# Kernel tuning notes

Hardware: AMD Instinct MI355X
Metric: run time of the kernel (lower is better)

## Reference

```python
import jax, jax.numpy as jnp
import numpy as np

NUM_LABELS = 512
MIN_INTENSITY = -0.003
MAX_INTENSITY = 0.003
BACKGROUND = 0


def setup_inputs() -> dict:
    key = jax.random.key(0)
    k1, k2 = jax.random.split(key)
    shape = (16, 1024, 1024)
    label_image = jax.random.randint(k1, shape, 0, NUM_LABELS, dtype=jnp.int32)
    intensity_image = jax.random.normal(k2, shape, dtype=jnp.float32)
    return {"label_image": label_image, "intensity_image": intensity_image}


def reference(label_image, intensity_image):
    # Single-pass segment reduce over all pixels, replacing the O(L*N) python loop.
    labels_flat = label_image.reshape(-1)
    vals_flat = intensity_image.reshape(-1)
    sums = jax.ops.segment_sum(vals_flat, labels_flat, num_segments=NUM_LABELS)
    counts = jax.ops.segment_sum(jnp.ones_like(vals_flat), labels_flat,
                                 num_segments=NUM_LABELS)
    means = sums / jnp.maximum(counts, 1.0)  # labels absent from image are never indexed
    label_ids = jnp.arange(NUM_LABELS, dtype=label_image.dtype)
    # Both min and max thresholds are set (truthy), background label is exempt.
    bad = ((means < MIN_INTENSITY) | (means > MAX_INTENSITY)) & (label_ids != BACKGROUND)
    # Threshold-based scatter filter: failing labels -> background.
    return jnp.where(bad[label_image], jnp.asarray(BACKGROUND, label_image.dtype), label_image)
```

## Files before the change

kernel.cpp:

```cpp
#include <hip/hip_runtime.h>

#define NUM_LABELS 512
#define MIN_INTENSITY (-0.003f)
#define MAX_INTENSITY (0.003f)


__global__ __launch_bounds__(256) void accum_kernel(
    const int* __restrict__ labels,
    const float* __restrict__ vals,
    float* __restrict__ g_sum,
    unsigned int* __restrict__ g_cnt,
    int n) {
  __shared__ float s_sum[NUM_LABELS];
  __shared__ unsigned int s_cnt[NUM_LABELS];
  for (int i = threadIdx.x; i < NUM_LABELS; i += blockDim.x) {
    s_sum[i] = 0.0f;
    s_cnt[i] = 0u;
  }
  __syncthreads();

  const int n4 = n >> 2;
  const int stride = gridDim.x * blockDim.x;
  int i = blockIdx.x * blockDim.x + threadIdx.x;
  const int4* l4 = reinterpret_cast<const int4*>(labels);
  const float4* v4 = reinterpret_cast<const float4*>(vals);
  for (; i < n4; i += stride) {
    int4 l = l4[i];
    float4 v = v4[i];
    atomicAdd(&s_sum[l.x], v.x); atomicAdd(&s_cnt[l.x], 1u);
    atomicAdd(&s_sum[l.y], v.y); atomicAdd(&s_cnt[l.y], 1u);
    atomicAdd(&s_sum[l.z], v.z); atomicAdd(&s_cnt[l.z], 1u);
    atomicAdd(&s_sum[l.w], v.w); atomicAdd(&s_cnt[l.w], 1u);
  }
  for (int t = (n4 << 2) + blockIdx.x * blockDim.x + threadIdx.x; t < n;
       t += stride) {
    atomicAdd(&s_sum[labels[t]], vals[t]);
    atomicAdd(&s_cnt[labels[t]], 1u);
  }
  __syncthreads();

  for (int j = threadIdx.x; j < NUM_LABELS; j += blockDim.x) {
    unsigned int c = s_cnt[j];
    if (c) {
      atomicAdd(&g_sum[j], s_sum[j]);
      atomicAdd(&g_cnt[j], c);
    }
  }
}

__global__ __launch_bounds__(NUM_LABELS) void flags_kernel(
    const float* __restrict__ g_sum,
    const unsigned int* __restrict__ g_cnt,
    int* __restrict__ bad) {
  int l = threadIdx.x;
  float c = (float)g_cnt[l];
  float mean = g_sum[l] / fmaxf(c, 1.0f);
  int b = ((mean < MIN_INTENSITY) || (mean > MAX_INTENSITY)) && (l != 0);
  bad[l] = b;
}

__global__ __launch_bounds__(256) void apply_kernel(
    const int* __restrict__ labels,
    const int* __restrict__ bad,
    int* __restrict__ out,
    int n) {
  __shared__ int s_bad[NUM_LABELS];
  for (int i = threadIdx.x; i < NUM_LABELS; i += blockDim.x)
    s_bad[i] = bad[i];
  __syncthreads();

  const int n4 = n >> 2;
  const int stride = gridDim.x * blockDim.x;
  int i = blockIdx.x * blockDim.x + threadIdx.x;
  const int4* l4 = reinterpret_cast<const int4*>(labels);
  int4* o4 = reinterpret_cast<int4*>(out);
  for (; i < n4; i += stride) {
    int4 l = l4[i];
    int4 o;
    o.x = s_bad[l.x] ? 0 : l.x;
    o.y = s_bad[l.y] ? 0 : l.y;
    o.z = s_bad[l.z] ? 0 : l.z;
    o.w = s_bad[l.w] ? 0 : l.w;
    o4[i] = o;
  }
  for (int t = (n4 << 2) + blockIdx.x * blockDim.x + threadIdx.x; t < n;
       t += stride) {
    int l = labels[t];
    out[t] = s_bad[l] ? 0 : l;
  }
}

extern "C" void kernel_launch(void* const* d_in, const int* in_sizes, int n_in,
                              void* d_out, int out_size, void* d_ws,
                              size_t ws_size, hipStream_t stream) {
  const int* labels = (const int*)d_in[0];
  const float* vals = (const float*)d_in[1];
  int* out = (int*)d_out;
  const int n = in_sizes[0];

  float* g_sum = (float*)d_ws;
  unsigned int* g_cnt = (unsigned int*)((char*)d_ws + NUM_LABELS * 4);
  int* bad = (int*)((char*)d_ws + NUM_LABELS * 8);

  hipMemsetAsync(d_ws, 0, NUM_LABELS * 8, stream);

  const int block = 256;
  int grid = (n / 4 + block - 1) / block;
  if (grid > 2048) grid = 2048;
  if (grid < 1) grid = 1;

  accum_kernel<<<grid, block, 0, stream>>>(labels, vals, g_sum, g_cnt, n);
  flags_kernel<<<1, NUM_LABELS, 0, stream>>>(g_sum, g_cnt, bad);
  apply_kernel<<<grid, block, 0, stream>>>(labels, bad, out, n);
}
```

Baseline: 233.0 us.

## Pack fixed-point sum and count into one 64-bit shared atomic per pixel

Replaces the separate float-sum and count shared atomics with a single 64-bit integer atomic. It carries a fixed-point sum in the high bits and the count in the low 25 bits, halving the LDS atomic traffic. The flags kernel is folded into the apply kernel prologue, saving one launch. Both loops are unrolled by four to get more loads in flight. Fixed-point quantization at 2^20 scale can shift means near the threshold, and 64-bit LDS atomics may themselves be slower than 32-bit float atomics.

```diff
diff --git a/kernel.cpp b/kernel.cpp
--- a/kernel.cpp
+++ b/kernel.cpp
@@ -1,90 +1,119 @@
 #include <hip/hip_runtime.h>
 
 #define NUM_LABELS 512
-#define MIN_INTENSITY (-0.003f)
-#define MAX_INTENSITY (0.003f)
+#define CNT_BITS 25
+#define CNT_MASK ((1LL << CNT_BITS) - 1)
+#define FXSCALE 1048576.0f
 
+__device__ __forceinline__ unsigned long long pack1(float v) {
+  long long fx = (long long)__float2int_rn(v * FXSCALE);
+  return (unsigned long long)(fx * (1LL << CNT_BITS) + 1LL);
+}
 
 __global__ __launch_bounds__(256) void accum_kernel(
     const int* __restrict__ labels,
     const float* __restrict__ vals,
-    float* __restrict__ g_sum,
-    unsigned int* __restrict__ g_cnt,
+    unsigned long long* __restrict__ g_hist,
     int n) {
-  __shared__ float s_sum[NUM_LABELS];
-  __shared__ unsigned int s_cnt[NUM_LABELS];
-  for (int i = threadIdx.x; i < NUM_LABELS; i += blockDim.x) {
-    s_sum[i] = 0.0f;
-    s_cnt[i] = 0u;
+  __shared__ unsigned long long s_hist[NUM_LABELS];
+  for (int i = threadIdx.x; i < NUM_LABELS; i += 256) s_hist[i] = 0ULL;
+  __syncthreads();
+
+  const int n4 = n >> 2;
+  const int tid = blockIdx.x * 256 + threadIdx.x;
+  const int stride = gridDim.x * 256;
+  const int4* l4 = reinterpret_cast<const int4*>(labels);
+  const float4* v4 = reinterpret_cast<const float4*>(vals);
+
+  for (int base = tid; base < n4; base += 4 * stride) {
+    const int i0 = base;
+    const int i1 = base + stride;
+    const int i2 = base + 2 * stride;
+    const int i3 = base + 3 * stride;
+    const bool p1 = i1 < n4, p2 = i2 < n4, p3 = i3 < n4;
+
+    int4 l0 = l4[i0];
+    float4 v0 = v4[i0];
+    int4 l1, l2, l3;
+    float4 v1, v2, v3;
+    if (p1) { l1 = l4[i1]; v1 = v4[i1]; }
+    if (p2) { l2 = l4[i2]; v2 = v4[i2]; }
+    if (p3) { l3 = l4[i3]; v3 = v4[i3]; }
+
+#define ACC4(L, V)                                   \
+    atomicAdd(&s_hist[(L).x], pack1((V).x));         \
+    atomicAdd(&s_hist[(L).y], pack1((V).y));         \
+    atomicAdd(&s_hist[(L).z], pack1((V).z));         \
+    atomicAdd(&s_hist[(L).w], pack1((V).w));
+
+    ACC4(l0, v0)
+    if (p1) { ACC4(l1, v1) }
+    if (p2) { ACC4(l2, v2) }
+    if (p3) { ACC4(l3, v3) }
+#undef ACC4
+  }
+
+  for (int t = (n4 << 2) + tid; t < n; t += stride) {
+    atomicAdd(&s_hist[labels[t]], pack1(vals[t]));
+  }
+  __syncthreads();
+
+  for (int j = threadIdx.x; j < NUM_LABELS; j += 256) {
+    unsigned long long h = s_hist[j];
+    if (h) atomicAdd(&g_hist[j], h);
+  }
+}
+
+__global__ __launch_bounds__(256) void apply_kernel(
+    const int* __restrict__ labels,
+    const unsigned long long* __restrict__ g_hist,
+    int* __restrict__ out,
+    int n) {
+  __shared__ int s_bad[NUM_LABELS];
+  for (int j = threadIdx.x; j < NUM_LABELS; j += 256) {
+    long long p = (long long)g_hist[j];
+    int cnt = (int)(p & CNT_MASK);
+    long long sf = p >> CNT_BITS;
+    int c = cnt > 1 ? cnt : 1;
+    float mean = (float)((double)sf / ((double)FXSCALE * (double)c));
+    s_bad[j] = ((mean < -0.003f) || (mean > 0.003f)) && (j != 0);
   }
   __syncthreads();
 
   const int n4 = n >> 2;
-  const int stride = gridDim.x * blockDim.x;
-  int i = blockIdx.x * blockDim.x + threadIdx.x;
-  const int4* l4 = reinterpret_cast<const int4*>(labels);
-  const float4* v4 = reinterpret_cast<const float4*>(vals);
-  for (; i < n4; i += stride) {
-    int4 l = l4[i];
-    float4 v = v4[i];
-    atomicAdd(&s_sum[l.x], v.x); atomicAdd(&s_cnt[l.x], 1u);
-    atomicAdd(&s_sum[l.y], v.y); atomicAdd(&s_cnt[l.y], 1u);
-    atomicAdd(&s_sum[l.z], v.z); atomicAdd(&s_cnt[l.z], 1u);
-    atomicAdd(&s_sum[l.w], v.w); atomicAdd(&s_cnt[l.w], 1u);
-  }
-  for (int t = (n4 << 2) + blockIdx.x * blockDim.x + threadIdx.x; t < n;
-       t += stride) {
-    atomicAdd(&s_sum[labels[t]], vals[t]);
-    atomicAdd(&s_cnt[labels[t]], 1u);
-  }
-  __syncthreads();
-
-  for (int j = threadIdx.x; j < NUM_LABELS; j += blockDim.x) {
-    unsigned int c = s_cnt[j];
-    if (c) {
-      atomicAdd(&g_sum[j], s_sum[j]);
-      atomicAdd(&g_cnt[j], c);
-    }
-  }
-}
-
-__global__ __launch_bounds__(NUM_LABELS) void flags_kernel(
-    const float* __restrict__ g_sum,
-    const unsigned int* __restrict__ g_cnt,
-    int* __restrict__ bad) {
-  int l = threadIdx.x;
-  float c = (float)g_cnt[l];
-  float mean = g_sum[l] / fmaxf(c, 1.0f);
-  int b = ((mean < MIN_INTENSITY) || (mean > MAX_INTENSITY)) && (l != 0);
-  bad[l] = b;
-}
-
-__global__ __launch_bounds__(256) void apply_kernel(
-    const int* __restrict__ labels,
-    const int* __restrict__ bad,
-    int* __restrict__ out,
-    int n) {
-  __shared__ int s_bad[NUM_LABELS];
-  for (int i = threadIdx.x; i < NUM_LABELS; i += blockDim.x)
-    s_bad[i] = bad[i];
-  __syncthreads();
-
-  const int n4 = n >> 2;
-  const int stride = gridDim.x * blockDim.x;
-  int i = blockIdx.x * blockDim.x + threadIdx.x;
+  const int tid = blockIdx.x * 256 + threadIdx.x;
+  const int stride = gridDim.x * 256;
   const int4* l4 = reinterpret_cast<const int4*>(labels);
   int4* o4 = reinterpret_cast<int4*>(out);
-  for (; i < n4; i += stride) {
-    int4 l = l4[i];
-    int4 o;
-    o.x = s_bad[l.x] ? 0 : l.x;
-    o.y = s_bad[l.y] ? 0 : l.y;
-    o.z = s_bad[l.z] ? 0 : l.z;
-    o.w = s_bad[l.w] ? 0 : l.w;
-    o4[i] = o;
+
+  for (int base = tid; base < n4; base += 4 * stride) {
+    const int i0 = base;
+    const int i1 = base + stride;
+    const int i2 = base + 2 * stride;
+    const int i3 = base + 3 * stride;
+    const bool p1 = i1 < n4, p2 = i2 < n4, p3 = i3 < n4;
+
+    int4 l0 = l4[i0];
+    int4 l1, l2, l3;
+    if (p1) l1 = l4[i1];
+    if (p2) l2 = l4[i2];
+    if (p3) l3 = l4[i3];
+
+#define FILT(L)                                      \
+    { (L).x = s_bad[(L).x] ? 0 : (L).x;              \
+      (L).y = s_bad[(L).y] ? 0 : (L).y;              \
+      (L).z = s_bad[(L).z] ? 0 : (L).z;              \
+      (L).w = s_bad[(L).w] ? 0 : (L).w; }
+
+    FILT(l0)
+    o4[i0] = l0;
+    if (p1) { FILT(l1) o4[i1] = l1; }
+    if (p2) { FILT(l2) o4[i2] = l2; }
+    if (p3) { FILT(l3) o4[i3] = l3; }
+#undef FILT
   }
-  for (int t = (n4 << 2) + blockIdx.x * blockDim.x + threadIdx.x; t < n;
-       t += stride) {
+
+  for (int t = (n4 << 2) + tid; t < n; t += stride) {
     int l = labels[t];
     out[t] = s_bad[l] ? 0 : l;
   }
@@ -98,18 +127,13 @@
   int* out = (int*)d_out;
   const int n = in_sizes[0];
 
-  float* g_sum = (float*)d_ws;
-  unsigned int* g_cnt = (unsigned int*)((char*)d_ws + NUM_LABELS * 4);
-  int* bad = (int*)((char*)d_ws + NUM_LABELS * 8);
+  unsigned long long* g_hist = (unsigned long long*)d_ws;
 
   hipMemsetAsync(d_ws, 0, NUM_LABELS * 8, stream);
 
   const int block = 256;
-  int grid = (n / 4 + block - 1) / block;
-  if (grid > 2048) grid = 2048;
-  if (grid < 1) grid = 1;
+  const int grid = 2048;
 
-  accum_kernel<<<grid, block, 0, stream>>>(labels, vals, g_sum, g_cnt, n);
-  flags_kernel<<<1, NUM_LABELS, 0, stream>>>(g_sum, g_cnt, bad);
-  apply_kernel<<<grid, block, 0, stream>>>(labels, bad, out, n);
+  accum_kernel<<<grid, block, 0, stream>>>(labels, vals, g_hist, n);
+  apply_kernel<<<grid, block, 0, stream>>>(labels, g_hist, out, n);
 }
```

Result: faster. 196.5 us (-15.7%).
